# Kernel tuning notes

Measured on AMD Instinct MI355X. Metric: run time of the kernel, lower is better.

## Reference

```python
import jax, jax.numpy as jnp
import numpy as np
from jax import lax

BETA = 0.25            # commitment_beta (multiplies code_book_loss per source)
CODEBOOK_WEIGHT = 1.0  # multiplies commitment_loss per source
GN_GROUPS = 8
GN_EPS = 1e-5


def conv2d(x, w, b):
    # 3x3 same-padding conv, NCHW / OIHW
    y = lax.conv_general_dilated(x, w, (1, 1), [(1, 1), (1, 1)],
                                 dimension_numbers=('NCHW', 'OIHW', 'NCHW'))
    return y + b[None, :, None, None]


def group_norm(x, scale, bias):
    B, C, H, W = x.shape
    xg = x.reshape(B, GN_GROUPS, C // GN_GROUPS, H, W)
    mean = xg.mean(axis=(2, 3, 4), keepdims=True)
    var = xg.var(axis=(2, 3, 4), keepdims=True)
    xg = (xg - mean) * lax.rsqrt(var + GN_EPS)
    x = xg.reshape(B, C, H, W)
    return x * scale[None, :, None, None] + bias[None, :, None, None]


def setup_inputs() -> dict:
    key = jax.random.key(0)
    ks = jax.random.split(key, 4)
    x = jax.random.normal(ks[0], (8, 3, 64, 64), jnp.float32)
    conv_in_w = jax.random.normal(ks[1], (64, 3, 3, 3), jnp.float32) * 0.1
    conv_in_b = jnp.zeros((64,), jnp.float32)
    codebook = jax.random.normal(ks[2], (4096, 64), jnp.float32) * 0.5
    gn_scale = jnp.ones((64,), jnp.float32)
    gn_bias = jnp.zeros((64,), jnp.float32)
    dec_w = jax.random.normal(ks[3], (3, 64, 3, 3), jnp.float32) * 0.1
    dec_b = jnp.zeros((3,), jnp.float32)
    return {"x": x, "conv_in_w": conv_in_w, "conv_in_b": conv_in_b,
            "codebook": codebook, "gn_scale": gn_scale, "gn_bias": gn_bias,
            "dec_w": dec_w, "dec_b": dec_b}


def reference(x, conv_in_w, conv_in_b, codebook, gn_scale, gn_bias, dec_w, dec_b):
    # Encoder: channels=[64], mid_layers=[64] => just conv_in
    feat = conv2d(x, conv_in_w, conv_in_b)          # [B,64,H,W]
    B, C, H, W = feat.shape

    # quantize(): cdist -> argmin -> gather -> losses -> straight-through
    quant_in = feat.transpose(0, 2, 3, 1).reshape(B, H * W, C)  # [B,n,C]
    # squared euclidean distances (argmin identical to torch.cdist p=2 argmin)
    d = ((quant_in ** 2).sum(-1, keepdims=True)
         - 2.0 * jnp.einsum('bnc,kc->bnk', quant_in, codebook)
         + (codebook ** 2).sum(-1)[None, None, :])              # [B,n,K]
    min_idx = jnp.argmin(d, axis=-1)                            # [B,n]
    quant_out = codebook[min_idx.reshape(-1)]                   # [B*n,C]
    qi_flat = quant_in.reshape(-1, C)                            # [B*n,C]

    commitment_loss = CODEBOOK_WEIGHT * jnp.mean(
        (lax.stop_gradient(quant_out) - qi_flat) ** 2)
    code_book_loss = BETA * jnp.mean(
        (lax.stop_gradient(qi_flat) - quant_out) ** 2)

    st = qi_flat + lax.stop_gradient(quant_out - qi_flat)        # straight-through
    quant_nchw = st.reshape(B, H, W, C).transpose(0, 3, 1, 2)

    # Decoder: channels=[64] => norm_out + silu + decoder_out
    out = group_norm(quant_nchw, gn_scale, gn_bias)
    out = jax.nn.silu(out)
    reconstruction = conv2d(out, dec_w, dec_b)                   # [B,3,H,W]
    return reconstruction, quant_nchw, commitment_loss, code_book_loss
```

## Files before the change

kernel.cpp:

```cpp
#include <hip/hip_runtime.h>
#include <hip/hip_bf16.h>

typedef __attribute__((ext_vector_type(8))) short short8;
typedef __attribute__((ext_vector_type(4))) float f32x4;

#define KK 4096
#define NELEM 2097152
#define TAU 2.5e-4f
#define RESCUE_CAP 8192

__device__ __forceinline__ unsigned short f2bf(float f) {
    unsigned u = __float_as_uint(f);
    u = (u + 0x7FFFu + ((u >> 16) & 1u)) >> 16;
    return (unsigned short)u;
}
__device__ __forceinline__ float bf2f(unsigned short h) {
    return __uint_as_float(((unsigned)h) << 16);
}

__global__ void k_prep(const float* __restrict__ cb, float* __restrict__ cn,
                       unsigned short* __restrict__ cbh, unsigned short* __restrict__ cbl) {
    int t = blockIdx.x * 256 + threadIdx.x;
    int row = t >> 2, part = t & 3;
    const float4* p = (const float4*)(cb + (size_t)row * 64 + part * 16);
    float s = 0.f;
    short8 hv[2], lv[2];
#pragma unroll
    for (int i = 0; i < 4; i++) {
        float4 v = p[i];
        float arr[4] = {v.x, v.y, v.z, v.w};
#pragma unroll
        for (int j = 0; j < 4; j++) {
            float f = arr[j];
            s += f * f;
            int e = i * 4 + j;
            unsigned short h = f2bf(f);
            hv[e >> 3][e & 7] = (short)h;
            lv[e >> 3][e & 7] = (short)f2bf(f - bf2f(h));
        }
    }
    short8* oh = (short8*)(cbh + (size_t)row * 64 + part * 16);
    short8* ol = (short8*)(cbl + (size_t)row * 64 + part * 16);
    oh[0] = hv[0]; oh[1] = hv[1];
    ol[0] = lv[0]; ol[1] = lv[1];
    s += __shfl_xor(s, 1, 64);
    s += __shfl_xor(s, 2, 64);
    if (part == 0) cn[row] = s;
}

#define MFMA __builtin_amdgcn_mfma_f32_16x16x32_bf16

__global__ __launch_bounds__(256, 2) void k_argmin_part(
    const float* __restrict__ x, const float* __restrict__ ciw, const float* __restrict__ cib,
    const unsigned short* __restrict__ cbh, const unsigned short* __restrict__ cbl,
    const float* __restrict__ cn,
    float* __restrict__ pb1, float* __restrict__ pb2, int* __restrict__ pbi) {

    __shared__ float    slab[3][3][66];
    __shared__ unsigned qtile[64][65];
    __shared__ float    mb1[4][64];
    __shared__ float    mb2[4][64];
    __shared__ int      mi1[4][64];

    const int tid = threadIdx.x;
    const int L   = tid & 63;
    const int wv  = tid >> 6;
    const int blk = blockIdx.x;
    const int grp = blk >> 1, half = blk & 1;
    const int b   = grp >> 6, h = grp & 63;

    for (int idx = tid; idx < 594; idx += 256) {
        int ci = idx / 198, rem = idx - ci * 198;
        int kh = rem / 66,  colp = rem - kh * 66;
        int hh = h + kh - 1, ww = colp - 1;
        float v = 0.f;
        if (hh >= 0 && hh < 64 && ww >= 0 && ww < 64)
            v = x[((b * 3 + ci) << 12) + (hh << 6) + ww];
        slab[ci][kh][colp] = v;
    }
    __syncthreads();

    {
        const int w_  = L;
        const int cgs = __builtin_amdgcn_readfirstlane(wv);
        float xv[27];
#pragma unroll
        for (int ci = 0; ci < 3; ci++)
#pragma unroll
            for (int kh = 0; kh < 3; kh++)
#pragma unroll
                for (int kw = 0; kw < 3; kw++)
                    xv[ci * 9 + kh * 3 + kw] = slab[ci][kh][w_ + kw];
#pragma unroll
        for (int j = 0; j < 16; j++) {
            int co = cgs * 16 + j;
            float acc = cib[co];
#pragma unroll
            for (int t2 = 0; t2 < 27; t2++)
                acc = fmaf(xv[t2], ciw[co * 27 + t2], acc);
            unsigned short hbits = f2bf(acc);
            unsigned short lbits = f2bf(acc - bf2f(hbits));
            qtile[w_][co] = (unsigned)hbits | ((unsigned)lbits << 16);
        }
    }
    __syncthreads();

    const int col = L & 15, g = L >> 4;
    short8 qh[4][2], ql[4][2];
#pragma unroll
    for (int mt = 0; mt < 4; mt++) {
        int qrow = mt * 16 + col;
#pragma unroll
        for (int kh = 0; kh < 2; kh++) {
            int d0 = (kh * 4 + g) * 8;
#pragma unroll
            for (int e = 0; e < 8; e++) {
                unsigned u = qtile[qrow][d0 + e];
                qh[mt][kh][e] = (short)(u & 0xFFFFu);
                ql[mt][kh][e] = (short)(u >> 16);
            }
        }
    }

    float vb1[4][4], vb2[4][4];
    int   vi1[4][4];
#pragma unroll
    for (int mt = 0; mt < 4; mt++)
#pragma unroll
        for (int e = 0; e < 4; e++) { vb1[mt][e] = 3.4e38f; vb2[mt][e] = 3.4e38f; vi1[mt][e] = 0; }

    const int cbase0 = (half << 11) + (wv << 9);
    const unsigned short* ph = cbh + (size_t)(cbase0 + col) * 64;
    const unsigned short* pl = cbl + (size_t)(cbase0 + col) * 64;
    const float* pcn = cn + cbase0 + col;

    short8 c0h0, c0h1, c0l0, c0l1, c1h0, c1h1, c1l0, c1l1;
    float  cn0, cn1;

    auto LD = [&](int gi, short8& h0, short8& h1, short8& l0, short8& l1, float& cnv) {
        const short8* p0 = (const short8*)(ph + ((size_t)gi << 10));
        const short8* p1 = (const short8*)(pl + ((size_t)gi << 10));
        h0 = p0[g]; h1 = p0[4 + g]; l0 = p1[g]; l1 = p1[4 + g];
        cnv = pcn[gi << 4];
    };
    auto PROC = [&](int gi, short8& h0, short8& h1, short8& l0, short8& l1, float cnv) {
        int kvb = cbase0 + gi * 16 + col;
#pragma unroll
        for (int mt = 0; mt < 4; mt++) {
            f32x4 acc = {0.f, 0.f, 0.f, 0.f};
            acc = MFMA(qh[mt][0], h0, acc, 0, 0, 0);
            acc = MFMA(qh[mt][1], h1, acc, 0, 0, 0);
            acc = MFMA(qh[mt][0], l0, acc, 0, 0, 0);
            acc = MFMA(qh[mt][1], l1, acc, 0, 0, 0);
            acc = MFMA(ql[mt][0], h0, acc, 0, 0, 0);
            acc = MFMA(ql[mt][1], h1, acc, 0, 0, 0);
#pragma unroll
            for (int e = 0; e < 4; e++) {
                float s = fmaf(acc[e], -2.f, cnv);
                vb2[mt][e] = __builtin_amdgcn_fmed3f(s, vb1[mt][e], vb2[mt][e]);
                bool take = s < vb1[mt][e];
                vi1[mt][e] = take ? kvb : vi1[mt][e];
                vb1[mt][e] = take ? s : vb1[mt][e];
            }
        }
    };

    LD(0, c0h0, c0h1, c0l0, c0l1, cn0);
#pragma unroll 1
    for (int gi = 0; gi < 32; gi += 2) {
        LD(gi + 1, c1h0, c1h1, c1l0, c1l1, cn1);
        PROC(gi, c0h0, c0h1, c0l0, c0l1, cn0);
        int gn = gi + 2 <= 31 ? gi + 2 : 31;
        LD(gn, c0h0, c0h1, c0l0, c0l1, cn0);
        PROC(gi + 1, c1h0, c1h1, c1l0, c1l1, cn1);
    }

#pragma unroll
    for (int mt = 0; mt < 4; mt++)
#pragma unroll
    for (int e = 0; e < 4; e++) {
        float b1 = vb1[mt][e], b2 = vb2[mt][e];
        int i1 = vi1[mt][e];
#pragma unroll
        for (int m = 1; m < 16; m <<= 1) {
            float ob1 = __shfl_xor(b1, m, 64);
            float ob2 = __shfl_xor(b2, m, 64);
            int   oi1 = __shfl_xor(i1, m, 64);
            float hi = fmaxf(b1, ob1);
            b2 = fminf(fminf(b2, ob2), hi);
            bool take = (ob1 < b1) || ((ob1 == b1) && (oi1 < i1));
            if (take) { b1 = ob1; i1 = oi1; }
        }
        if (col == 0) {
            int qloc = mt * 16 + g * 4 + e;
            mb1[wv][qloc] = b1; mb2[wv][qloc] = b2; mi1[wv][qloc] = i1;
        }
    }
    __syncthreads();

    if (tid < 64) {
        float b1 = mb1[0][tid], b2 = mb2[0][tid];
        int i1 = mi1[0][tid];
#pragma unroll
        for (int w2 = 1; w2 < 4; w2++) {
            float ob1 = mb1[w2][tid], ob2 = mb2[w2][tid];
            int   oi1 = mi1[w2][tid];
            float hi = fmaxf(b1, ob1);
            b2 = fminf(fminf(b2, ob2), hi);
            bool take = (ob1 < b1) || ((ob1 == b1) && (oi1 < i1));
            if (take) { b1 = ob1; i1 = oi1; }
        }
        int o = (blk << 6) + tid;
        pb1[o] = b1; pb2[o] = b2; pbi[o] = i1;
    }
}

__global__ __launch_bounds__(256, 2) void k_merge(
    const float* __restrict__ x, const float* __restrict__ ciw, const float* __restrict__ cib,
    const float* __restrict__ cb,
    const float* __restrict__ pb1, const float* __restrict__ pb2, const int* __restrict__ pbi,
    float* __restrict__ quant, float* __restrict__ ssd,
    float* __restrict__ gsum, float* __restrict__ gsq,
    unsigned int* __restrict__ rcnt, int* __restrict__ rlist) {

    __shared__ float    slab[3][3][66];
    __shared__ unsigned qtile[64][65];
    __shared__ int      fi[64];
    __shared__ float    gred[4][16];

    const int tid = threadIdx.x;
    const int L   = tid & 63;
    const int wv  = tid >> 6;
    const int grp = blockIdx.x;
    const int b   = grp >> 6, h = grp & 63;

    for (int idx = tid; idx < 594; idx += 256) {
        int ci = idx / 198, rem = idx - ci * 198;
        int kh = rem / 66,  colp = rem - kh * 66;
        int hh = h + kh - 1, ww = colp - 1;
        float v = 0.f;
        if (hh >= 0 && hh < 64 && ww >= 0 && ww < 64)
            v = x[((b * 3 + ci) << 12) + (hh << 6) + ww];
        slab[ci][kh][colp] = v;
    }
    __syncthreads();
    {
        const int w_  = L;
        const int cgs = __builtin_amdgcn_readfirstlane(wv);
        float xv[27];
#pragma unroll
        for (int ci = 0; ci < 3; ci++)
#pragma unroll
            for (int kh = 0; kh < 3; kh++)
#pragma unroll
                for (int kw = 0; kw < 3; kw++)
                    xv[ci * 9 + kh * 3 + kw] = slab[ci][kh][w_ + kw];
#pragma unroll
        for (int j = 0; j < 16; j++) {
            int co = cgs * 16 + j;
            float acc = cib[co];
#pragma unroll
            for (int t2 = 0; t2 < 27; t2++)
                acc = fmaf(xv[t2], ciw[co * 27 + t2], acc);
            unsigned short hbits = f2bf(acc);
            unsigned short lbits = f2bf(acc - bf2f(hbits));
            qtile[w_][co] = (unsigned)hbits | ((unsigned)lbits << 16);
        }
    }
    __syncthreads();

    if (tid < 64) {
        int i0 = (grp << 7) + tid;
        int j0 = i0 + 64;
        float b1 = pb1[i0], b2 = pb2[i0];
        int   i1 = pbi[i0];
        float ob1 = pb1[j0], ob2 = pb2[j0];
        int   oi1 = pbi[j0];
        float hi = fmaxf(b1, ob1);
        b2 = fminf(fminf(b2, ob2), hi);
        bool take = (ob1 < b1) || ((ob1 == b1) && (oi1 < i1));
        if (take) { b1 = ob1; i1 = oi1; }
        fi[tid] = i1;
        if (b2 - b1 < TAU) {
            unsigned pos = atomicAdd(rcnt, 1u);
            if (pos < RESCUE_CAP) {
                rlist[2 * pos] = (grp << 6) + tid;
                rlist[2 * pos + 1] = i1;
            }
        }
    }
    __syncthreads();

    {
        int qloc = tid >> 2, part = tid & 3;
        int idx = fi[qloc];
        int q = (grp << 6) + qloc;
        int hw = q & 4095;
        const float* crow = cb + (size_t)idx * 64 + part * 16;
        float* qout = quant + ((size_t)b << 18) + ((size_t)(part * 16) << 12) + hw;
        float ps = 0.f, sA = 0.f, sA2 = 0.f, sB = 0.f, sB2 = 0.f;
#pragma unroll
        for (int cc = 0; cc < 16; cc++) {
            unsigned u = qtile[qloc][part * 16 + cc];
            float fv = bf2f((unsigned short)(u & 0xFFFFu)) + bf2f((unsigned short)(u >> 16));
            float cv = crow[cc];
            float d = cv - fv;
            ps += d * d;
            if (cc < 8) { sA += cv; sA2 += cv * cv; } else { sB += cv; sB2 += cv * cv; }
            qout[(size_t)cc << 12] = cv;
        }
#pragma unroll
        for (int off = 32; off; off >>= 1) ps += __shfl_down(ps, off, 64);
        if (L == 0) atomicAdd(ssd, ps);
#pragma unroll
        for (int m = 4; m <= 32; m <<= 1) {
            sA  += __shfl_xor(sA, m, 64);  sA2 += __shfl_xor(sA2, m, 64);
            sB  += __shfl_xor(sB, m, 64);  sB2 += __shfl_xor(sB2, m, 64);
        }
        if (L < 4) {
            gred[wv][L * 4 + 0] = sA;  gred[wv][L * 4 + 1] = sA2;
            gred[wv][L * 4 + 2] = sB;  gred[wv][L * 4 + 3] = sB2;
        }
    }
    __syncthreads();
    if (tid < 16) {
        float v = gred[0][tid] + gred[1][tid] + gred[2][tid] + gred[3][tid];
        int part = tid >> 2, stat = tid & 3;
        int g2 = b * 8 + part * 2 + (stat >> 1);
        atomicAdd((stat & 1) ? &gsq[g2] : &gsum[g2], v);
    }
}

__global__ void k_rescue(const int* __restrict__ rlist, const unsigned int* __restrict__ rcnt,
                         const float* __restrict__ x, const float* __restrict__ ciw,
                         const float* __restrict__ cib,
                         const float* __restrict__ cb, const float* __restrict__ cn,
                         float* __restrict__ quant, float* __restrict__ ssd,
                         float* __restrict__ gsum, float* __restrict__ gsq) {
    __shared__ float fqs[64];
    __shared__ float rb[4];
    __shared__ int   ri[4];
    __shared__ int   s_new;
    int tid = threadIdx.x;
    unsigned cnt = *rcnt;
    int n = (int)(cnt > RESCUE_CAP ? RESCUE_CAP : cnt);
    for (int r = blockIdx.x; r < n; r += gridDim.x) {
        int q = rlist[2 * r], old_i = rlist[2 * r + 1];
        int b = q >> 12, h = (q >> 6) & 63, w_ = q & 63;
        if (tid < 64) {
            float acc = cib[tid];
#pragma unroll
            for (int ci = 0; ci < 3; ci++)
#pragma unroll
            for (int kh = 0; kh < 3; kh++) {
                int hh = h + kh - 1;
                if (hh < 0 || hh >= 64) continue;
#pragma unroll
                for (int kw = 0; kw < 3; kw++) {
                    int ww = w_ + kw - 1;
                    if (ww < 0 || ww >= 64) continue;
                    acc = fmaf(x[((b * 3 + ci) << 12) + (hh << 6) + ww],
                               ciw[tid * 27 + ci * 9 + kh * 3 + kw], acc);
                }
            }
            fqs[tid] = acc;
        }
        __syncthreads();
        float best = 3.4e38f; int bi = 0;
        for (int kk = 0; kk < 16; kk++) {
            int k = kk * 256 + tid;
            const float4* cp = (const float4*)(cb + (size_t)k * 64);
            float d0 = 0.f, d1 = 0.f, d2 = 0.f, d3 = 0.f;
#pragma unroll
            for (int i = 0; i < 16; i += 4) {
                float4 c0 = cp[i], c1 = cp[i+1], c2 = cp[i+2], c3 = cp[i+3];
                d0 += fqs[4*i+ 0]*c0.x + fqs[4*i+ 1]*c0.y + fqs[4*i+ 2]*c0.z + fqs[4*i+ 3]*c0.w;
                d1 += fqs[4*i+ 4]*c1.x + fqs[4*i+ 5]*c1.y + fqs[4*i+ 6]*c1.z + fqs[4*i+ 7]*c1.w;
                d2 += fqs[4*i+ 8]*c2.x + fqs[4*i+ 9]*c2.y + fqs[4*i+10]*c2.z + fqs[4*i+11]*c2.w;
                d3 += fqs[4*i+12]*c3.x + fqs[4*i+13]*c3.y + fqs[4*i+14]*c3.z + fqs[4*i+15]*c3.w;
            }
            float s = cn[k] - 2.f * ((d0 + d1) + (d2 + d3));
            if (s < best) { best = s; bi = k; }
        }
#pragma unroll
        for (int off = 32; off; off >>= 1) {
            float ob = __shfl_down(best, off, 64);
            int   oi = __shfl_down(bi, off, 64);
            if (ob < best || (ob == best && oi < bi)) { best = ob; bi = oi; }
        }
        if ((tid & 63) == 0) { rb[tid >> 6] = best; ri[tid >> 6] = bi; }
        __syncthreads();
        if (tid == 0) {
            float bb = rb[0]; int ii = ri[0];
#pragma unroll
            for (int w2 = 1; w2 < 4; w2++)
                if (rb[w2] < bb || (rb[w2] == bb && ri[w2] < ii)) { bb = rb[w2]; ii = ri[w2]; }
            s_new = ii;
        }
        __syncthreads();
        int ni = s_new;
        if (ni != old_i && tid < 64) {
            float fv = fqs[tid];
            float co_ = cb[(size_t)old_i * 64 + tid];
            float cw  = cb[(size_t)ni * 64 + tid];
            quant[((size_t)b << 18) + ((size_t)tid << 12) + (q & 4095)] = cw;
            float dssd = (cw - fv) * (cw - fv) - (co_ - fv) * (co_ - fv);
            float ds  = cw - co_;
            float ds2 = cw * cw - co_ * co_;
#pragma unroll
            for (int off = 32; off; off >>= 1) dssd += __shfl_down(dssd, off, 64);
#pragma unroll
            for (int m = 1; m < 8; m <<= 1) {
                ds  += __shfl_xor(ds, m, 64);
                ds2 += __shfl_xor(ds2, m, 64);
            }
            if (tid == 0) atomicAdd(ssd, dssd);
            if ((tid & 7) == 0) {
                atomicAdd(&gsum[b * 8 + (tid >> 3)], ds);
                atomicAdd(&gsq [b * 8 + (tid >> 3)], ds2);
            }
        }
        __syncthreads();
    }
}

__global__ __launch_bounds__(256, 2) void k_out(
    const float* __restrict__ quant,
    const float* __restrict__ gsum, const float* __restrict__ gsq,
    const float* __restrict__ scale, const float* __restrict__ bias,
    const float* __restrict__ dw, const float* __restrict__ db,
    float* __restrict__ out) {

    __shared__ float nls[64 * 3 * 66];
    __shared__ float sc_s[64], bi_s[64];

    const int tid = threadIdx.x;
    const int blk = blockIdx.x;
    const int b = blk >> 6, h = blk & 63;

    if (tid < 64) {
        int grp = b * 8 + (tid >> 3);
        float m = gsum[grp] * (1.f / 32768.f);
        float var = gsq[grp] * (1.f / 32768.f) - m * m;
        float r = rsqrtf(var + 1e-5f);
        float sc = scale[tid] * r;
        sc_s[tid] = sc;
        bi_s[tid] = bias[tid] - m * sc;
    }
    for (int idx = tid; idx < 384; idx += 256) {
        int ci = idx / 6, r2 = idx % 6;
        int kh = r2 >> 1, side = r2 & 1;
        nls[ci * 198 + kh * 66 + (side ? 65 : 0)] = 0.f;
    }
    __syncthreads();

#pragma unroll
    for (int i = 0; i < 48; i++) {
        int idx = tid + i * 256;
        int w_ = idx & 63;
        int t2 = idx >> 6;
        int kh = t2 % 3, ci = t2 / 3;
        int hh = h + kh - 1;
        float v = 0.f;
        if (hh >= 0 && hh < 64) {
            float qv = quant[((size_t)(b * 64 + ci) << 12) + (hh << 6) + w_];
            float y = qv * sc_s[ci] + bi_s[ci];
            v = y / (1.f + expf(-y));
        }
        nls[ci * 198 + kh * 66 + w_ + 1] = v;
    }
    __syncthreads();

    const int co = tid >> 6;
    const int w_ = tid & 63;
    if (co < 3) {
        float acc = db[co];
#pragma unroll 4
        for (int ci = 0; ci < 64; ci++) {
            const float* wt = dw + (size_t)(co * 64 + ci) * 9;
#pragma unroll
            for (int kh = 0; kh < 3; kh++) {
                const float* base = nls + ci * 198 + kh * 66 + w_;
                acc = fmaf(base[0], wt[kh * 3 + 0], acc);
                acc = fmaf(base[1], wt[kh * 3 + 1], acc);
                acc = fmaf(base[2], wt[kh * 3 + 2], acc);
            }
        }
        out[((size_t)(b * 3 + co) << 12) + (h << 6) + w_] = acc;
    }
}

__global__ void k_loss(const float* __restrict__ ssd, float* __restrict__ losses) {
    float mean = ssd[0] / 2097152.f;
    losses[0] = mean;
    losses[1] = 0.25f * mean;
}

extern "C" void kernel_launch(void* const* d_in, const int* in_sizes, int n_in,
                              void* d_out, int out_size, void* d_ws, size_t ws_size,
                              hipStream_t stream) {
    const float* x   = (const float*)d_in[0];
    const float* ciw = (const float*)d_in[1];
    const float* cib = (const float*)d_in[2];
    const float* cb  = (const float*)d_in[3];
    const float* gsc = (const float*)d_in[4];
    const float* gbi = (const float*)d_in[5];
    const float* dw  = (const float*)d_in[6];
    const float* db  = (const float*)d_in[7];

    float* out = (float*)d_out;
    char* wsb  = (char*)d_ws;

    float*          ssd   = (float*)wsb;
    unsigned int*   rcnt  = (unsigned int*)(wsb + 4);
    float*          gsum  = (float*)(wsb + 64);
    float*          gsq   = (float*)(wsb + 320);
    float*          cn    = (float*)(wsb + 1024);
    int*            rlist = (int*)(wsb + 65536);
    unsigned short* cbh   = (unsigned short*)(wsb + 131072);
    unsigned short* cbl   = (unsigned short*)(wsb + 655360);
    float*          pb1   = (float*)(wsb + 1179648);
    float*          pb2   = (float*)(wsb + 1441792);
    int*            pbi   = (int*)(wsb + 1703936);

    float* recon  = out;
    float* quant  = out + 98304;
    float* losses = out + 98304 + NELEM;

    hipMemsetAsync(wsb, 0, 1024, stream);
    k_prep        <<<64,   256, 0, stream>>>(cb, cn, cbh, cbl);
    k_argmin_part <<<1024, 256, 0, stream>>>(x, ciw, cib, cbh, cbl, cn, pb1, pb2, pbi);
    k_merge       <<<512,  256, 0, stream>>>(x, ciw, cib, cb, pb1, pb2, pbi,
                                             quant, ssd, gsum, gsq, rcnt, rlist);
    k_rescue      <<<256,  256, 0, stream>>>(rlist, rcnt, x, ciw, cib, cb, cn,
                                             quant, ssd, gsum, gsq);
    k_out         <<<512,  256, 0, stream>>>(quant, gsum, gsq, gsc, gbi, dw, db, recon);
    k_loss        <<<1,    1,   0, stream>>>(ssd, losses);
}
```

Before: 273.4 us.

## Fuse merge into argmin via last-block ticket and drop memset and loss launches

```diff
diff --git a/kernel.cpp b/kernel.cpp
--- a/kernel.cpp
+++ b/kernel.cpp
@@ -19,7 +19,11 @@
 }
 
 __global__ void k_prep(const float* __restrict__ cb, float* __restrict__ cn,
-                       unsigned short* __restrict__ cbh, unsigned short* __restrict__ cbl) {
+                       unsigned short* __restrict__ cbh, unsigned short* __restrict__ cbl,
+                       int* __restrict__ wszero) {
+    if (blockIdx.x == 0) {
+        for (int i = threadIdx.x; i < 768; i += 256) wszero[i] = 0;
+    }
     int t = blockIdx.x * 256 + threadIdx.x;
     int row = t >> 2, part = t & 3;
     const float4* p = (const float4*)(cb + (size_t)row * 64 + part * 16);
@@ -50,17 +54,24 @@
 
 #define MFMA __builtin_amdgcn_mfma_f32_16x16x32_bf16
 
-__global__ __launch_bounds__(256, 2) void k_argmin_part(
+__global__ __launch_bounds__(256, 2) void k_argmin(
     const float* __restrict__ x, const float* __restrict__ ciw, const float* __restrict__ cib,
     const unsigned short* __restrict__ cbh, const unsigned short* __restrict__ cbl,
-    const float* __restrict__ cn,
-    float* __restrict__ pb1, float* __restrict__ pb2, int* __restrict__ pbi) {
+    const float* __restrict__ cn, const float* __restrict__ cb,
+    float* __restrict__ pb1, float* __restrict__ pb2, int* __restrict__ pbi,
+    int* __restrict__ ticket,
+    float* __restrict__ quant, float* __restrict__ ssd,
+    float* __restrict__ gsum, float* __restrict__ gsq,
+    unsigned int* __restrict__ rcnt, int* __restrict__ rlist) {
 
     __shared__ float    slab[3][3][66];
     __shared__ unsigned qtile[64][65];
     __shared__ float    mb1[4][64];
     __shared__ float    mb2[4][64];
     __shared__ int      mi1[4][64];
+    __shared__ int      fi[64];
+    __shared__ float    gred[4][16];
+    __shared__ int      sold;
 
     const int tid = threadIdx.x;
     const int L   = tid & 63;
@@ -213,61 +224,13 @@
         int o = (blk << 6) + tid;
         pb1[o] = b1; pb2[o] = b2; pbi[o] = i1;
     }
-}
-
-__global__ __launch_bounds__(256, 2) void k_merge(
-    const float* __restrict__ x, const float* __restrict__ ciw, const float* __restrict__ cib,
-    const float* __restrict__ cb,
-    const float* __restrict__ pb1, const float* __restrict__ pb2, const int* __restrict__ pbi,
-    float* __restrict__ quant, float* __restrict__ ssd,
-    float* __restrict__ gsum, float* __restrict__ gsq,
-    unsigned int* __restrict__ rcnt, int* __restrict__ rlist) {
-
-    __shared__ float    slab[3][3][66];
-    __shared__ unsigned qtile[64][65];
-    __shared__ int      fi[64];
-    __shared__ float    gred[4][16];
-
-    const int tid = threadIdx.x;
-    const int L   = tid & 63;
-    const int wv  = tid >> 6;
-    const int grp = blockIdx.x;
-    const int b   = grp >> 6, h = grp & 63;
-
-    for (int idx = tid; idx < 594; idx += 256) {
-        int ci = idx / 198, rem = idx - ci * 198;
-        int kh = rem / 66,  colp = rem - kh * 66;
-        int hh = h + kh - 1, ww = colp - 1;
-        float v = 0.f;
-        if (hh >= 0 && hh < 64 && ww >= 0 && ww < 64)
-            v = x[((b * 3 + ci) << 12) + (hh << 6) + ww];
-        slab[ci][kh][colp] = v;
-    }
-    __syncthreads();
-    {
-        const int w_  = L;
-        const int cgs = __builtin_amdgcn_readfirstlane(wv);
-        float xv[27];
-#pragma unroll
-        for (int ci = 0; ci < 3; ci++)
-#pragma unroll
-            for (int kh = 0; kh < 3; kh++)
-#pragma unroll
-                for (int kw = 0; kw < 3; kw++)
-                    xv[ci * 9 + kh * 3 + kw] = slab[ci][kh][w_ + kw];
-#pragma unroll
-        for (int j = 0; j < 16; j++) {
-            int co = cgs * 16 + j;
-            float acc = cib[co];
-#pragma unroll
-            for (int t2 = 0; t2 < 27; t2++)
-                acc = fmaf(xv[t2], ciw[co * 27 + t2], acc);
-            unsigned short hbits = f2bf(acc);
-            unsigned short lbits = f2bf(acc - bf2f(hbits));
-            qtile[w_][co] = (unsigned)hbits | ((unsigned)lbits << 16);
-        }
-    }
-    __syncthreads();
+    __syncthreads();
+
+    __threadfence();
+    if (tid == 0) sold = atomicAdd(&ticket[grp], 1);
+    __syncthreads();
+    if (sold != 1) return;
+    __threadfence();
 
     if (tid < 64) {
         int i0 = (grp << 7) + tid;
@@ -429,6 +392,7 @@
     const float* __restrict__ gsum, const float* __restrict__ gsq,
     const float* __restrict__ scale, const float* __restrict__ bias,
     const float* __restrict__ dw, const float* __restrict__ db,
+    const float* __restrict__ ssd, float* __restrict__ losses,
     float* __restrict__ out) {
 
     __shared__ float nls[64 * 3 * 66];
@@ -437,6 +401,12 @@
     const int tid = threadIdx.x;
     const int blk = blockIdx.x;
     const int b = blk >> 6, h = blk & 63;
+
+    if (blk == 0 && tid == 0) {
+        float mean = ssd[0] / 2097152.f;
+        losses[0] = mean;
+        losses[1] = 0.25f * mean;
+    }
 
     if (tid < 64) {
         int grp = b * 8 + (tid >> 3);
@@ -490,12 +460,6 @@
     }
 }
 
-__global__ void k_loss(const float* __restrict__ ssd, float* __restrict__ losses) {
-    float mean = ssd[0] / 2097152.f;
-    losses[0] = mean;
-    losses[1] = 0.25f * mean;
-}
-
 extern "C" void kernel_launch(void* const* d_in, const int* in_sizes, int n_in,
                               void* d_out, int out_size, void* d_ws, size_t ws_size,
                               hipStream_t stream) {
@@ -511,29 +475,29 @@
     float* out = (float*)d_out;
     char* wsb  = (char*)d_ws;
 
-    float*          ssd   = (float*)wsb;
-    unsigned int*   rcnt  = (unsigned int*)(wsb + 4);
-    float*          gsum  = (float*)(wsb + 64);
-    float*          gsq   = (float*)(wsb + 320);
-    float*          cn    = (float*)(wsb + 1024);
-    int*            rlist = (int*)(wsb + 65536);
-    unsigned short* cbh   = (unsigned short*)(wsb + 131072);
-    unsigned short* cbl   = (unsigned short*)(wsb + 655360);
-    float*          pb1   = (float*)(wsb + 1179648);
-    float*          pb2   = (float*)(wsb + 1441792);
-    int*            pbi   = (int*)(wsb + 1703936);
+    float*          ssd    = (float*)wsb;
+    unsigned int*   rcnt   = (unsigned int*)(wsb + 4);
+    float*          gsum   = (float*)(wsb + 64);
+    float*          gsq    = (float*)(wsb + 320);
+    int*            ticket = (int*)(wsb + 1024);
+    float*          cn     = (float*)(wsb + 4096);
+    int*            rlist  = (int*)(wsb + 65536);
+    unsigned short* cbh    = (unsigned short*)(wsb + 131072);
+    unsigned short* cbl    = (unsigned short*)(wsb + 655360);
+    float*          pb1    = (float*)(wsb + 1179648);
+    float*          pb2    = (float*)(wsb + 1441792);
+    int*            pbi    = (int*)(wsb + 1703936);
 
     float* recon  = out;
     float* quant  = out + 98304;
     float* losses = out + 98304 + NELEM;
 
-    hipMemsetAsync(wsb, 0, 1024, stream);
-    k_prep        <<<64,   256, 0, stream>>>(cb, cn, cbh, cbl);
-    k_argmin_part <<<1024, 256, 0, stream>>>(x, ciw, cib, cbh, cbl, cn, pb1, pb2, pbi);
-    k_merge       <<<512,  256, 0, stream>>>(x, ciw, cib, cb, pb1, pb2, pbi,
-                                             quant, ssd, gsum, gsq, rcnt, rlist);
-    k_rescue      <<<256,  256, 0, stream>>>(rlist, rcnt, x, ciw, cib, cb, cn,
-                                             quant, ssd, gsum, gsq);
-    k_out         <<<512,  256, 0, stream>>>(quant, gsum, gsq, gsc, gbi, dw, db, recon);
-    k_loss        <<<1,    1,   0, stream>>>(ssd, losses);
-}
+    k_prep   <<<64,   256, 0, stream>>>(cb, cn, cbh, cbl, (int*)wsb);
+    k_argmin <<<1024, 256, 0, stream>>>(x, ciw, cib, cbh, cbl, cn, cb,
+                                        pb1, pb2, pbi, ticket,
+                                        quant, ssd, gsum, gsq, rcnt, rlist);
+    k_rescue <<<256,  256, 0, stream>>>(rlist, rcnt, x, ciw, cib, cb, cn,
+                                        quant, ssd, gsum, gsq);
+    k_out    <<<512,  256, 0, stream>>>(quant, gsum, gsq, gsc, gbi, dw, db,
+                                        ssd, losses, recon);
+}
```

After: 361.2 us. 1.32x slower.

## Fold near-tie rescue into merge kernel and drop memset and loss launches

Applied to the files above, without the earlier changes.

```diff
diff --git a/kernel.cpp b/kernel.cpp
--- a/kernel.cpp
+++ b/kernel.cpp
@@ -7,7 +7,6 @@
 #define KK 4096
 #define NELEM 2097152
 #define TAU 2.5e-4f
-#define RESCUE_CAP 8192
 
 __device__ __forceinline__ unsigned short f2bf(float f) {
     unsigned u = __float_as_uint(f);
@@ -19,7 +18,11 @@
 }
 
 __global__ void k_prep(const float* __restrict__ cb, float* __restrict__ cn,
-                       unsigned short* __restrict__ cbh, unsigned short* __restrict__ cbl) {
+                       unsigned short* __restrict__ cbh, unsigned short* __restrict__ cbl,
+                       int* __restrict__ wszero) {
+    if (blockIdx.x == 0) {
+        for (int i = threadIdx.x; i < 256; i += 256) wszero[i] = 0;
+    }
     int t = blockIdx.x * 256 + threadIdx.x;
     int row = t >> 2, part = t & 3;
     const float4* p = (const float4*)(cb + (size_t)row * 64 + part * 16);
@@ -217,16 +220,19 @@
 
 __global__ __launch_bounds__(256, 2) void k_merge(
     const float* __restrict__ x, const float* __restrict__ ciw, const float* __restrict__ cib,
-    const float* __restrict__ cb,
+    const float* __restrict__ cb, const float* __restrict__ cn,
     const float* __restrict__ pb1, const float* __restrict__ pb2, const int* __restrict__ pbi,
     float* __restrict__ quant, float* __restrict__ ssd,
-    float* __restrict__ gsum, float* __restrict__ gsq,
-    unsigned int* __restrict__ rcnt, int* __restrict__ rlist) {
-
-    __shared__ float    slab[3][3][66];
-    __shared__ unsigned qtile[64][65];
-    __shared__ int      fi[64];
-    __shared__ float    gred[4][16];
+    float* __restrict__ gsum, float* __restrict__ gsq) {
+
+    __shared__ float slab[3][3][66];
+    __shared__ float qf32[64][65];
+    __shared__ int   fi[64];
+    __shared__ float gred[4][16];
+    __shared__ int   nflag;
+    __shared__ int   flagged[64];
+    __shared__ float rb[4];
+    __shared__ int   ri[4];
 
     const int tid = threadIdx.x;
     const int L   = tid & 63;
@@ -234,6 +240,7 @@
     const int grp = blockIdx.x;
     const int b   = grp >> 6, h = grp & 63;
 
+    if (tid == 0) nflag = 0;
     for (int idx = tid; idx < 594; idx += 256) {
         int ci = idx / 198, rem = idx - ci * 198;
         int kh = rem / 66,  colp = rem - kh * 66;
@@ -262,9 +269,7 @@
 #pragma unroll
             for (int t2 = 0; t2 < 27; t2++)
                 acc = fmaf(xv[t2], ciw[co * 27 + t2], acc);
-            unsigned short hbits = f2bf(acc);
-            unsigned short lbits = f2bf(acc - bf2f(hbits));
-            qtile[w_][co] = (unsigned)hbits | ((unsigned)lbits << 16);
+            qf32[w_][co] = acc;
         }
     }
     __syncthreads();
@@ -282,14 +287,48 @@
         if (take) { b1 = ob1; i1 = oi1; }
         fi[tid] = i1;
         if (b2 - b1 < TAU) {
-            unsigned pos = atomicAdd(rcnt, 1u);
-            if (pos < RESCUE_CAP) {
-                rlist[2 * pos] = (grp << 6) + tid;
-                rlist[2 * pos + 1] = i1;
+            int p = atomicAdd(&nflag, 1);
+            flagged[p] = tid;
+        }
+    }
+    __syncthreads();
+
+    int nf = nflag;
+    for (int r = 0; r < nf; r++) {
+        int qf = flagged[r];
+        float best = 3.4e38f; int bi = 0;
+        for (int kk = 0; kk < 16; kk++) {
+            int k = kk * 256 + tid;
+            const float4* cp = (const float4*)(cb + (size_t)k * 64);
+            float d0 = 0.f, d1 = 0.f, d2 = 0.f, d3 = 0.f;
+#pragma unroll
+            for (int i = 0; i < 16; i += 4) {
+                float4 c0 = cp[i], c1 = cp[i+1], c2 = cp[i+2], c3 = cp[i+3];
+                d0 += qf32[qf][4*i+ 0]*c0.x + qf32[qf][4*i+ 1]*c0.y + qf32[qf][4*i+ 2]*c0.z + qf32[qf][4*i+ 3]*c0.w;
+                d1 += qf32[qf][4*i+ 4]*c1.x + qf32[qf][4*i+ 5]*c1.y + qf32[qf][4*i+ 6]*c1.z + qf32[qf][4*i+ 7]*c1.w;
+                d2 += qf32[qf][4*i+ 8]*c2.x + qf32[qf][4*i+ 9]*c2.y + qf32[qf][4*i+10]*c2.z + qf32[qf][4*i+11]*c2.w;
+                d3 += qf32[qf][4*i+12]*c3.x + qf32[qf][4*i+13]*c3.y + qf32[qf][4*i+14]*c3.z + qf32[qf][4*i+15]*c3.w;
             }
-        }
-    }
-    __syncthreads();
+            float s = cn[k] - 2.f * ((d0 + d1) + (d2 + d3));
+            if (s < best) { best = s; bi = k; }
+        }
+#pragma unroll
+        for (int off = 32; off; off >>= 1) {
+            float ob = __shfl_down(best, off, 64);
+            int   oi = __shfl_down(bi, off, 64);
+            if (ob < best || (ob == best && oi < bi)) { best = ob; bi = oi; }
+        }
+        if (L == 0) { rb[wv] = best; ri[wv] = bi; }
+        __syncthreads();
+        if (tid == 0) {
+            float bb = rb[0]; int ii = ri[0];
+#pragma unroll
+            for (int w2 = 1; w2 < 4; w2++)
+                if (rb[w2] < bb || (rb[w2] == bb && ri[w2] < ii)) { bb = rb[w2]; ii = ri[w2]; }
+            fi[qf] = ii;
+        }
+        __syncthreads();
+    }
 
     {
         int qloc = tid >> 2, part = tid & 3;
@@ -301,8 +340,7 @@
         float ps = 0.f, sA = 0.f, sA2 = 0.f, sB = 0.f, sB2 = 0.f;
 #pragma unroll
         for (int cc = 0; cc < 16; cc++) {
-            unsigned u = qtile[qloc][part * 16 + cc];
-            float fv = bf2f((unsigned short)(u & 0xFFFFu)) + bf2f((unsigned short)(u >> 16));
+            float fv = qf32[qloc][part * 16 + cc];
             float cv = crow[cc];
             float d = cv - fv;
             ps += d * d;
@@ -331,104 +369,12 @@
     }
 }
 
-__global__ void k_rescue(const int* __restrict__ rlist, const unsigned int* __restrict__ rcnt,
-                         const float* __restrict__ x, const float* __restrict__ ciw,
-                         const float* __restrict__ cib,
-                         const float* __restrict__ cb, const float* __restrict__ cn,
-                         float* __restrict__ quant, float* __restrict__ ssd,
-                         float* __restrict__ gsum, float* __restrict__ gsq) {
-    __shared__ float fqs[64];
-    __shared__ float rb[4];
-    __shared__ int   ri[4];
-    __shared__ int   s_new;
-    int tid = threadIdx.x;
-    unsigned cnt = *rcnt;
-    int n = (int)(cnt > RESCUE_CAP ? RESCUE_CAP : cnt);
-    for (int r = blockIdx.x; r < n; r += gridDim.x) {
-        int q = rlist[2 * r], old_i = rlist[2 * r + 1];
-        int b = q >> 12, h = (q >> 6) & 63, w_ = q & 63;
-        if (tid < 64) {
-            float acc = cib[tid];
-#pragma unroll
-            for (int ci = 0; ci < 3; ci++)
-#pragma unroll
-            for (int kh = 0; kh < 3; kh++) {
-                int hh = h + kh - 1;
-                if (hh < 0 || hh >= 64) continue;
-#pragma unroll
-                for (int kw = 0; kw < 3; kw++) {
-                    int ww = w_ + kw - 1;
-                    if (ww < 0 || ww >= 64) continue;
-                    acc = fmaf(x[((b * 3 + ci) << 12) + (hh << 6) + ww],
-                               ciw[tid * 27 + ci * 9 + kh * 3 + kw], acc);
-                }
-            }
-            fqs[tid] = acc;
-        }
-        __syncthreads();
-        float best = 3.4e38f; int bi = 0;
-        for (int kk = 0; kk < 16; kk++) {
-            int k = kk * 256 + tid;
-            const float4* cp = (const float4*)(cb + (size_t)k * 64);
-            float d0 = 0.f, d1 = 0.f, d2 = 0.f, d3 = 0.f;
-#pragma unroll
-            for (int i = 0; i < 16; i += 4) {
-                float4 c0 = cp[i], c1 = cp[i+1], c2 = cp[i+2], c3 = cp[i+3];
-                d0 += fqs[4*i+ 0]*c0.x + fqs[4*i+ 1]*c0.y + fqs[4*i+ 2]*c0.z + fqs[4*i+ 3]*c0.w;
-                d1 += fqs[4*i+ 4]*c1.x + fqs[4*i+ 5]*c1.y + fqs[4*i+ 6]*c1.z + fqs[4*i+ 7]*c1.w;
-                d2 += fqs[4*i+ 8]*c2.x + fqs[4*i+ 9]*c2.y + fqs[4*i+10]*c2.z + fqs[4*i+11]*c2.w;
-                d3 += fqs[4*i+12]*c3.x + fqs[4*i+13]*c3.y + fqs[4*i+14]*c3.z + fqs[4*i+15]*c3.w;
-            }
-            float s = cn[k] - 2.f * ((d0 + d1) + (d2 + d3));
-            if (s < best) { best = s; bi = k; }
-        }
-#pragma unroll
-        for (int off = 32; off; off >>= 1) {
-            float ob = __shfl_down(best, off, 64);
-            int   oi = __shfl_down(bi, off, 64);
-            if (ob < best || (ob == best && oi < bi)) { best = ob; bi = oi; }
-        }
-        if ((tid & 63) == 0) { rb[tid >> 6] = best; ri[tid >> 6] = bi; }
-        __syncthreads();
-        if (tid == 0) {
-            float bb = rb[0]; int ii = ri[0];
-#pragma unroll
-            for (int w2 = 1; w2 < 4; w2++)
-                if (rb[w2] < bb || (rb[w2] == bb && ri[w2] < ii)) { bb = rb[w2]; ii = ri[w2]; }
-            s_new = ii;
-        }
-        __syncthreads();
-        int ni = s_new;
-        if (ni != old_i && tid < 64) {
-            float fv = fqs[tid];
-            float co_ = cb[(size_t)old_i * 64 + tid];
-            float cw  = cb[(size_t)ni * 64 + tid];
-            quant[((size_t)b << 18) + ((size_t)tid << 12) + (q & 4095)] = cw;
-            float dssd = (cw - fv) * (cw - fv) - (co_ - fv) * (co_ - fv);
-            float ds  = cw - co_;
-            float ds2 = cw * cw - co_ * co_;
-#pragma unroll
-            for (int off = 32; off; off >>= 1) dssd += __shfl_down(dssd, off, 64);
-#pragma unroll
-            for (int m = 1; m < 8; m <<= 1) {
-                ds  += __shfl_xor(ds, m, 64);
-                ds2 += __shfl_xor(ds2, m, 64);
-            }
-            if (tid == 0) atomicAdd(ssd, dssd);
-            if ((tid & 7) == 0) {
-                atomicAdd(&gsum[b * 8 + (tid >> 3)], ds);
-                atomicAdd(&gsq [b * 8 + (tid >> 3)], ds2);
-            }
-        }
-        __syncthreads();
-    }
-}
-
 __global__ __launch_bounds__(256, 2) void k_out(
     const float* __restrict__ quant,
     const float* __restrict__ gsum, const float* __restrict__ gsq,
     const float* __restrict__ scale, const float* __restrict__ bias,
     const float* __restrict__ dw, const float* __restrict__ db,
+    const float* __restrict__ ssd, float* __restrict__ losses,
     float* __restrict__ out) {
 
     __shared__ float nls[64 * 3 * 66];
@@ -437,6 +383,12 @@
     const int tid = threadIdx.x;
     const int blk = blockIdx.x;
     const int b = blk >> 6, h = blk & 63;
+
+    if (blk == 0 && tid == 0) {
+        float mean = ssd[0] / 2097152.f;
+        losses[0] = mean;
+        losses[1] = 0.25f * mean;
+    }
 
     if (tid < 64) {
         int grp = b * 8 + (tid >> 3);
@@ -490,12 +442,6 @@
     }
 }
 
-__global__ void k_loss(const float* __restrict__ ssd, float* __restrict__ losses) {
-    float mean = ssd[0] / 2097152.f;
-    losses[0] = mean;
-    losses[1] = 0.25f * mean;
-}
-
 extern "C" void kernel_launch(void* const* d_in, const int* in_sizes, int n_in,
                               void* d_out, int out_size, void* d_ws, size_t ws_size,
                               hipStream_t stream) {
@@ -511,29 +457,24 @@
     float* out = (float*)d_out;
     char* wsb  = (char*)d_ws;
 
-    float*          ssd   = (float*)wsb;
-    unsigned int*   rcnt  = (unsigned int*)(wsb + 4);
-    float*          gsum  = (float*)(wsb + 64);
-    float*          gsq   = (float*)(wsb + 320);
-    float*          cn    = (float*)(wsb + 1024);
-    int*            rlist = (int*)(wsb + 65536);
-    unsigned short* cbh   = (unsigned short*)(wsb + 131072);
-    unsigned short* cbl   = (unsigned short*)(wsb + 655360);
-    float*          pb1   = (float*)(wsb + 1179648);
-    float*          pb2   = (float*)(wsb + 1441792);
-    int*            pbi   = (int*)(wsb + 1703936);
+    float*          ssd  = (float*)wsb;
+    float*          gsum = (float*)(wsb + 64);
+    float*          gsq  = (float*)(wsb + 320);
+    float*          cn   = (float*)(wsb + 4096);
+    unsigned short* cbh  = (unsigned short*)(wsb + 131072);
+    unsigned short* cbl  = (unsigned short*)(wsb + 655360);
+    float*          pb1  = (float*)(wsb + 1179648);
+    float*          pb2  = (float*)(wsb + 1441792);
+    int*            pbi  = (int*)(wsb + 1703936);
 
     float* recon  = out;
     float* quant  = out + 98304;
     float* losses = out + 98304 + NELEM;
 
-    hipMemsetAsync(wsb, 0, 1024, stream);
-    k_prep        <<<64,   256, 0, stream>>>(cb, cn, cbh, cbl);
+    k_prep        <<<64,   256, 0, stream>>>(cb, cn, cbh, cbl, (int*)wsb);
     k_argmin_part <<<1024, 256, 0, stream>>>(x, ciw, cib, cbh, cbl, cn, pb1, pb2, pbi);
-    k_merge       <<<512,  256, 0, stream>>>(x, ciw, cib, cb, pb1, pb2, pbi,
-                                             quant, ssd, gsum, gsq, rcnt, rlist);
-    k_rescue      <<<256,  256, 0, stream>>>(rlist, rcnt, x, ciw, cib, cb, cn,
+    k_merge       <<<512,  256, 0, stream>>>(x, ciw, cib, cb, cn, pb1, pb2, pbi,
                                              quant, ssd, gsum, gsq);
-    k_out         <<<512,  256, 0, stream>>>(quant, gsum, gsq, gsc, gbi, dw, db, recon);
-    k_loss        <<<1,    1,   0, stream>>>(ssd, losses);
-}
+    k_out         <<<512,  256, 0, stream>>>(quant, gsum, gsq, gsc, gbi, dw, db,
+                                             ssd, losses, recon);
+}
```

Result: slower. 289.6 us (+5.9%).
